# Kernel tuning notes

Measured on AMD Instinct MI355X. Metric: run time of the kernel, lower is better.

Reference implementation:

```python
import jax, jax.numpy as jnp
import numpy as np

B = 65536
NE = 256   # n_encode
NH = 256   # n_hidden
NC = 4     # n_command
D = 64     # n_depth (BatchNorm channels)
F = 32     # n_features
M = D * (F // 2)  # 1024
EPS = 1e-5


def setup_inputs() -> dict:
    key = jax.random.key(0)
    ks = jax.random.split(key, 8)
    s = 0.05
    return {
        "feature": jax.random.normal(ks[0], (B, NE), jnp.float32),
        "hidden":  jax.random.normal(ks[1], (B, NH), jnp.float32),
        "command": jax.random.normal(ks[2], (B, NC), jnp.float32),
        # linear weights (torch Linear stores [out, in]); xavier-like scale
        "Wq":  jax.random.normal(ks[3], (D, NC), jnp.float32) * s,
        "Wkz": jax.random.normal(ks[4], (M, NE), jnp.float32) * s,
        "Wkh": jax.random.normal(ks[5], (M, NH), jnp.float32) * s,
        "Wvz": jax.random.normal(ks[6], (M, NE), jnp.float32) * s,
        "Wvh": jax.random.normal(ks[7], (M, NH), jnp.float32) * s,
        # BatchNorm1d(64) affine params (normV exists in __init__ but is unused)
        "gammaQ": jnp.ones((D,), jnp.float32),
        "betaQ":  jnp.zeros((D,), jnp.float32),
        "gammaK": jnp.ones((D,), jnp.float32),
        "betaK":  jnp.zeros((D,), jnp.float32),
    }


def reference(feature, hidden, command, Wq, Wkz, Wkh, Wvz, Wvh,
              gammaQ, betaQ, gammaK, betaK):
    # Q projection: [B, D]; BatchNorm1d over batch (training-mode batch stats,
    # biased variance, matching torch).
    Q = command @ Wq.T
    mQ = jnp.mean(Q, axis=0)
    vQ = jnp.mean(jnp.square(Q - mQ), axis=0)
    Qn = (Q - mQ) / jnp.sqrt(vQ + EPS) * gammaQ + betaQ          # [B, D]

    # K: cat([B,M],[B,M]) -> [B, 2M] -> view [B, F, D] -> transpose -> [B, D, F]
    K = jnp.concatenate([feature @ Wkz.T, hidden @ Wkh.T], axis=1)
    K = K.reshape(-1, F, D).transpose(0, 2, 1)                    # [B, D, F]
    mK = jnp.mean(K, axis=(0, 2), keepdims=True)
    vK = jnp.mean(jnp.square(K - mK), axis=(0, 2), keepdims=True)
    Kn = (K - mK) / jnp.sqrt(vK + EPS) * gammaK[None, :, None] + betaK[None, :, None]

    # V: [B, F, D], NOT batch-normed (normV is dead code in the original)
    V = jnp.concatenate([feature @ Wvz.T, hidden @ Wvh.T], axis=1).reshape(-1, F, D)

    # attention: [B,1,D] @ [B,D,F] -> [B,F] scores; softmax over F; then @ V
    A = jax.nn.softmax(jnp.einsum('bd,bdf->bf', Qn, Kn) / np.sqrt(D).astype(np.float32), axis=-1)
    s = jnp.einsum('bf,bfd->bd', A, V)                            # [B, D]
    return s
```

## Files before the change

### kernel.cpp

```cpp
#include <hip/hip_runtime.h>
#include <hip/hip_bf16.h>
#include <math.h>


typedef float  f32x4   __attribute__((ext_vector_type(4)));
typedef float  f32x16  __attribute__((ext_vector_type(16)));
typedef __bf16 bf16x4  __attribute__((ext_vector_type(4)));
typedef __bf16 bf16x8  __attribute__((ext_vector_type(8)));

#define MFMA16(A, B, C) __builtin_amdgcn_mfma_f32_16x16x32_bf16((A), (B), (C), 0, 0, 0)
#define MFMA32(A, B, C) __builtin_amdgcn_mfma_f32_32x32x16_bf16((A), (B), (C), 0, 0, 0)

#define EPSV 1e-5f

#define WS_WV    0x000000u
#define WS_WKF   0x100000u
#define WS_G     0x120000u
#define WS_CS    0x1A0000u
#define WS_CMDP  0x1A0800u
#define WS_T     0x1A1800u
#define WS_U     0x1A3800u
#define WS_WQ2   0x1A5800u
#define WS_C0    0x1A5C00u

__device__ __forceinline__ void gl_lds16(const void* g, void* l)
{
    __builtin_amdgcn_global_load_lds(
        (const __attribute__((address_space(1))) unsigned int*)g,
        (__attribute__((address_space(3))) unsigned int*)l, 16, 0, 0);
}

__global__ __launch_bounds__(512, 2) void setup1(const float* __restrict__ feat,
        const float* __restrict__ hid, const float4* __restrict__ cmd,
        const float* __restrict__ Wvz, const float* __restrict__ Wvh,
        __bf16* __restrict__ WV, float* __restrict__ CMDP, float* __restrict__ CS,
        __bf16* __restrict__ Gp)
{
    __shared__ __bf16 T[256 * 40];
    __shared__ float sm[8][14];
    const int blk = blockIdx.x;
    const int tid = threadIdx.x;

    if (blk >= 384) {
        const int b2 = blk - 384;
        float v[14];
#pragma unroll
        for (int k = 0; k < 14; ++k) v[k] = 0.f;
#pragma unroll
        for (int i = 0; i < 4; ++i) {
            float4 c = cmd[(b2 * 4 + i) * 512 + tid];
            v[0] += c.x;  v[1] += c.y;  v[2] += c.z;  v[3] += c.w;
            v[4] += c.x*c.x; v[5] += c.x*c.y; v[6] += c.x*c.z; v[7] += c.x*c.w;
            v[8] += c.y*c.y; v[9] += c.y*c.z; v[10] += c.y*c.w;
            v[11] += c.z*c.z; v[12] += c.z*c.w; v[13] += c.w*c.w;
        }
#pragma unroll
        for (int k = 0; k < 14; ++k) {
            float s = v[k];
#pragma unroll
            for (int off = 32; off; off >>= 1) s += __shfl_xor(s, off);
            if ((tid & 63) == 0) sm[tid >> 6][k] = s;
        }
        __syncthreads();
        if (tid < 14) {
            float s = 0.f;
#pragma unroll
            for (int w = 0; w < 8; ++w) s += sm[w][tid];
            CMDP[b2 * 14 + tid] = s;
        }
        return;
    }
    if (blk >= 128) {
        int t = (blk - 128) * 512 + tid;
        int e = t * 4;
        const float* src = (e < 262144) ? (Wvz + e) : (Wvh + (e - 262144));
        float4 a = *(const float4*)src;
        bf16x4 vv = { (__bf16)a.x, (__bf16)a.y, (__bf16)a.z, (__bf16)a.w };
        *(bf16x4*)(WV + e) = vv;
        return;
    }

    const int mat  = blk >> 6;
    const int chunk = blk & 63;
    const float* X = mat ? hid : feat;
    float* cs = CS + mat * 256;
    const int k0   = chunk * 1024;
    const int wid  = tid >> 6, lane = tid & 63, quad = lane >> 4, l15 = lane & 15;
    const int c    = tid & 255;
    const int t8   = tid >> 8;

    f32x4 acc[2][16];
#pragma unroll
    for (int mt = 0; mt < 2; ++mt)
#pragma unroll
        for (int nt = 0; nt < 16; ++nt) acc[mt][nt] = (f32x4){0.f, 0.f, 0.f, 0.f};

    float clsum = 0.f;
    for (int it = 0; it < 32; ++it) {
        __syncthreads();
        const int kb = k0 + it * 32;
#pragma unroll
        for (int i = 0; i < 16; ++i) {
            int k = t8 + 2 * i;
            float x = X[(size_t)(kb + k) * 256 + c];
            clsum += x;
            T[c * 40 + k] = (__bf16)x;
        }
        __syncthreads();
        bf16x8 a0 = *(const bf16x8*)&T[(wid * 32 +      l15) * 40 + quad * 8];
        bf16x8 a1 = *(const bf16x8*)&T[(wid * 32 + 16 + l15) * 40 + quad * 8];
#pragma unroll
        for (int nt = 0; nt < 16; ++nt) {
            bf16x8 b = *(const bf16x8*)&T[(nt * 16 + l15) * 40 + quad * 8];
            acc[0][nt] = MFMA16(a0, b, acc[0][nt]);
            acc[1][nt] = MFMA16(a1, b, acc[1][nt]);
        }
    }
    atomicAdd(&cs[c], clsum);
    __bf16* outp = Gp + (size_t)blk * 65536;
#pragma unroll
    for (int mt = 0; mt < 2; ++mt)
#pragma unroll
        for (int nt = 0; nt < 16; ++nt)
#pragma unroll
            for (int r = 0; r < 4; ++r) {
                int gi = wid * 32 + mt * 16 + quad * 4 + r;
                int gj = nt * 16 + l15;
                outp[gi * 256 + gj] = (__bf16)acc[mt][nt][r];
            }
}

__global__ void gram_reduce(const __bf16* __restrict__ Gp, float* __restrict__ G)
{
    int o = blockIdx.x * 256 + threadIdx.x;
    int mat = o >> 16, e = o & 65535;
    const __bf16* p = Gp + (size_t)mat * 64 * 65536 + e;
    float s = 0.f;
#pragma unroll 8
    for (int c = 0; c < 64; ++c) s += (float)p[(size_t)c * 65536];
    G[o] = s;
}

__global__ void rowstats(const float* __restrict__ Wkz, const float* __restrict__ Wkh,
        const float* __restrict__ G, const float* __restrict__ CS,
        float* __restrict__ Tout, float* __restrict__ Uout)
{
    const int blk = blockIdx.x;
    const int mat = blk >> 7, jg = blk & 127;
    const float* Wsrc = (mat ? Wkh : Wkz) + (size_t)jg * 8 * 256;
    const float* Gm = G + (size_t)mat * 65536;
    const float* cs = CS + mat * 256;
    __shared__ float wlT[256 * 8];
    __shared__ float red[4][16];
    const int tid = threadIdx.x, wid = tid >> 6, lane = tid & 63;
#pragma unroll
    for (int jj = 0; jj < 8; ++jj) wlT[tid * 8 + jj] = Wsrc[jj * 256 + tid];
    __syncthreads();
    float inner[8];
#pragma unroll
    for (int jj = 0; jj < 8; ++jj) inner[jj] = 0.f;
    for (int r = 0; r < 256; ++r) {
        float g = Gm[r * 256 + tid];
        float4 w0 = *(const float4*)&wlT[r * 8];
        float4 w1 = *(const float4*)&wlT[r * 8 + 4];
        inner[0] = fmaf(w0.x, g, inner[0]); inner[1] = fmaf(w0.y, g, inner[1]);
        inner[2] = fmaf(w0.z, g, inner[2]); inner[3] = fmaf(w0.w, g, inner[3]);
        inner[4] = fmaf(w1.x, g, inner[4]); inner[5] = fmaf(w1.y, g, inner[5]);
        inner[6] = fmaf(w1.z, g, inner[6]); inner[7] = fmaf(w1.w, g, inner[7]);
    }
    float cst = cs[tid];
#pragma unroll
    for (int jj = 0; jj < 8; ++jj) {
        float wme = wlT[tid * 8 + jj];
        float p = wme * inner[jj];
        float u = wme * cst;
#pragma unroll
        for (int off = 32; off; off >>= 1) { p += __shfl_xor(p, off); u += __shfl_xor(u, off); }
        if (lane == 0) { red[wid][jj] = p; red[wid][jj + 8] = u; }
    }
    __syncthreads();
    if (tid < 16) {
        float s = red[0][tid] + red[1][tid] + red[2][tid] + red[3][tid];
        int jj = tid & 7;
        int j = mat * 1024 + jg * 8 + jj;
        if (tid < 8) Tout[j] = s; else Uout[j] = s;
    }
}

__global__ void finalize_kernel(const float* __restrict__ Wq,
        const float* __restrict__ gQ, const float* __restrict__ bQ,
        const float* __restrict__ gK, const float* __restrict__ bK,
        const float* __restrict__ CMDP, const float* __restrict__ T,
        const float* __restrict__ U, float* __restrict__ Wq2, float* __restrict__ C0)
{
    __shared__ float s14[14];
    const int d = threadIdx.x;
    if (d < 14) {
        float s = 0.f;
        for (int b = 0; b < 32; ++b) s += CMDP[b * 14 + d];
        s14[d] = s;
    }
    __syncthreads();
    float s4[4] = { s14[0], s14[1], s14[2], s14[3] };
    float gc[4][4];
    gc[0][0] = s14[4];
    gc[0][1] = gc[1][0] = s14[5];
    gc[0][2] = gc[2][0] = s14[6];
    gc[0][3] = gc[3][0] = s14[7];
    gc[1][1] = s14[8];
    gc[1][2] = gc[2][1] = s14[9];
    gc[1][3] = gc[3][1] = s14[10];
    gc[2][2] = s14[11];
    gc[2][3] = gc[3][2] = s14[12];
    gc[3][3] = s14[13];
    float wq[4];
#pragma unroll
    for (int c = 0; c < 4; ++c) wq[c] = Wq[d * 4 + c];
    const float invB = 1.0f / 65536.0f;
    float mQ = (wq[0]*s4[0] + wq[1]*s4[1] + wq[2]*s4[2] + wq[3]*s4[3]) * invB;
    float eq2 = 0.f;
#pragma unroll
    for (int c = 0; c < 4; ++c)
#pragma unroll
        for (int c2 = 0; c2 < 4; ++c2) eq2 += wq[c] * wq[c2] * gc[c][c2];
    eq2 *= invB;
    float vQ  = eq2 - mQ * mQ;
    float aQ  = gQ[d] / sqrtf(vQ + EPSV);
    float bQv = bQ[d] - mQ * aQ;
    float S2 = 0.f, S1 = 0.f;
#pragma unroll
    for (int f = 0; f < 32; ++f) { S2 += T[f * 64 + d]; S1 += U[f * 64 + d]; }
    const float invBF = 1.0f / (65536.0f * 32.0f);
    float e2 = S2 * invBF, mK = S1 * invBF;
    float vK = e2 - mK * mK;
    float aK = gK[d] / sqrtf(vK + EPSV);
    float c1 = aQ * aK * 0.125f;
    C0[d] = bQv * aK * 0.125f;
#pragma unroll
    for (int c = 0; c < 4; ++c) Wq2[d * 4 + c] = c1 * wq[c];
}

__global__ void foldK(const float* __restrict__ Wkz, const float* __restrict__ Wkh,
                      const float* __restrict__ Wq2, const float* __restrict__ C0,
                      __bf16* __restrict__ WKF)
{
    const int blk = blockIdx.x;
    const int h = blk / 96, rr = blk % 96;
    const int k = threadIdx.x;
    float s = 0.f;
    if (rr < 80) {
        const int c = rr >> 4, fl = rr & 15;
        const float* Wsrc = (h ? Wkh : Wkz) + (size_t)fl * 64 * 256;
        for (int d = 0; d < 64; ++d) {
            float coef = (c == 0) ? C0[d] : Wq2[d * 4 + (c - 1)];
            s = fmaf(coef, Wsrc[d * 256 + k], s);
        }
    }
    WKF[(size_t)(h * 96 + rr) * 256 + k] = (__bf16)s;
}

__global__ __launch_bounds__(256, 2) void fused_attn(
        const float* __restrict__ feat, const float* __restrict__ hid,
        const float4* __restrict__ cmd, const __bf16* __restrict__ WV,
        const __bf16* __restrict__ WKF, float* __restrict__ out)
{
    __shared__ __bf16 BUF[32768];
    __shared__ __bf16 WGTs[16 * 128];
    const int tid  = threadIdx.x;
    const int wid  = tid >> 6, lane = tid & 63;
    const int l5   = lane & 31, hi = lane >> 5;
    const int fl   = l5 & 15;
    const bool low = (l5 < 16);
    const int wrow = (blockIdx.x << 7) + (wid << 5);

    int voff[12];
#pragma unroll
    for (int i = 0; i < 12; ++i) {
        int n = (wid << 1) + (i << 3) + hi;
        voff[i] = n * 256 + ((l5 ^ (n & 7)) << 3);
    }

    float l_i[16];
    f32x16 s_acc[2];
#pragma unroll
    for (int r = 0; r < 16; ++r) { l_i[r] = 0.f; s_acc[0][r] = 0.f; s_acc[1][r] = 0.f; }

    for (int h = 0; h < 2; ++h) {
        const float* X = h ? hid : feat;
        const __bf16* Wkf = WKF + ((size_t)h * 96 << 8);

        bf16x8 a2[16];
#pragma unroll
        for (int u = 0; u < 16; ++u) {
            const float* p = X + ((size_t)(wrow + l5) << 8) + u * 16 + hi * 8;
            float4 x0 = *(const float4*)p;
            float4 x1 = *(const float4*)(p + 4);
            a2[u] = (bf16x8){ (__bf16)x0.x, (__bf16)x0.y, (__bf16)x0.z, (__bf16)x0.w,
                              (__bf16)x1.x, (__bf16)x1.y, (__bf16)x1.z, (__bf16)x1.w };
        }

        __syncthreads();
#pragma unroll
        for (int i = 0; i < 12; ++i)
            gl_lds16(Wkf + voff[i], &BUF[((wid << 1) + (i << 3)) << 8]);
        __syncthreads();

        f32x16 acc1[3];
#pragma unroll
        for (int nt = 0; nt < 3; ++nt)
#pragma unroll
            for (int r = 0; r < 16; ++r) acc1[nt][r] = 0.f;
        __builtin_amdgcn_s_setprio(1);
#pragma unroll
        for (int ks = 0; ks < 16; ++ks)
#pragma unroll
            for (int nt = 0; nt < 3; ++nt) {
                int n = nt * 32 + l5;
                bf16x8 b = *(const bf16x8*)&BUF[n * 256 + (((ks * 2 + hi) ^ (n & 7)) << 3)];
                acc1[nt] = MFMA32(a2[ks], b, acc1[nt]);
            }
        __builtin_amdgcn_s_setprio(0);

#pragma unroll
        for (int g = 0; g < 4; ++g) {
            bf16x4 wv4;
#pragma unroll
            for (int j = 0; j < 4; ++j) {
                const int r = g * 4 + j;
                const int row32 = j + 8 * g + 4 * hi;
                float4 cm = cmd[wrow + row32];
                float e0, e1, t0[3], t1[3];
#pragma unroll
                for (int nt = 0; nt < 3; ++nt) {
                    e0 = acc1[nt][r];
                    e1 = __shfl_xor(e0, 16);
                    t0[nt] = low ? e0 : e1;
                    t1[nt] = low ? e1 : e0;
                }
                float sc = t0[0] + cm.x * t1[0] + cm.y * t0[1]
                                 + cm.z * t1[1] + cm.w * t0[2];
                float w = __expf(sc);
                wv4[j] = (__bf16)w;
                float ws = w;
                ws += __shfl_xor(ws, 1); ws += __shfl_xor(ws, 2);
                ws += __shfl_xor(ws, 4); ws += __shfl_xor(ws, 8);
                l_i[r] += ws;
            }
            if (low) *(bf16x4*)&WGTs[fl * 128 + (wid << 5) + 8 * g + 4 * hi] = wv4;
        }

        __syncthreads();

        {
            const __bf16* base = WV + ((size_t)(h * 16) << 14);
#pragma unroll
            for (int i = 0; i < 8; ++i)
                gl_lds16(base + voff[i], &BUF[((wid << 1) + (i << 3)) << 8]);
        }

        for (int f2 = 0; f2 < 16; ++f2) {
            const int bufsel = (f2 & 1) << 14;
            __syncthreads();
            if (f2 < 15) {
                const __bf16* base = WV + ((size_t)(h * 16 + f2 + 1) << 14);
                const int nsel = bufsel ^ 16384;
#pragma unroll
                for (int i = 0; i < 8; ++i)
                    gl_lds16(base + voff[i], &BUF[nsel + ((((wid << 1) + (i << 3))) << 8)]);
            }
            __builtin_amdgcn_sched_barrier(0);
            f32x16 acc2[2];
#pragma unroll
            for (int r = 0; r < 16; ++r) { acc2[0][r] = 0.f; acc2[1][r] = 0.f; }
            __builtin_amdgcn_s_setprio(1);
#pragma unroll
            for (int ks = 0; ks < 16; ++ks)
#pragma unroll
                for (int nt = 0; nt < 2; ++nt) {
                    int n = nt * 32 + l5;
                    bf16x8 b = *(const bf16x8*)&BUF[bufsel + n * 256
                                                    + (((ks * 2 + hi) ^ (n & 7)) << 3)];
                    acc2[nt] = MFMA32(a2[ks], b, acc2[nt]);
                }
            __builtin_amdgcn_s_setprio(0);
#pragma unroll
            for (int g = 0; g < 4; ++g) {
                bf16x4 wv = *(const bf16x4*)&WGTs[f2 * 128 + (wid << 5) + 8 * g + 4 * hi];
#pragma unroll
                for (int j = 0; j < 4; ++j) {
                    float w = (float)wv[j];
                    s_acc[0][g * 4 + j] += w * acc2[0][g * 4 + j];
                    s_acc[1][g * 4 + j] += w * acc2[1][g * 4 + j];
                }
            }
        }
    }

#pragma unroll
    for (int g = 0; g < 4; ++g)
#pragma unroll
        for (int j = 0; j < 4; ++j) {
            const int r = g * 4 + j;
            float inv = 1.0f / l_i[r];
            size_t row = (size_t)(wrow + j + 8 * g + 4 * hi);
            out[(row << 6) + l5]      = s_acc[0][r] * inv;
            out[(row << 6) + 32 + l5] = s_acc[1][r] * inv;
        }
}

extern "C" void kernel_launch(void* const* d_in, const int* in_sizes, int n_in,
                              void* d_out, int out_size, void* d_ws, size_t ws_size,
                              hipStream_t stream)
{
    (void)in_sizes; (void)n_in; (void)out_size; (void)ws_size;
    const float* feature = (const float*)d_in[0];
    const float* hidden  = (const float*)d_in[1];
    const float* command = (const float*)d_in[2];
    const float* Wq      = (const float*)d_in[3];
    const float* Wkz     = (const float*)d_in[4];
    const float* Wkh     = (const float*)d_in[5];
    const float* Wvz     = (const float*)d_in[6];
    const float* Wvh     = (const float*)d_in[7];
    const float* gammaQ  = (const float*)d_in[8];
    const float* betaQ   = (const float*)d_in[9];
    const float* gammaK  = (const float*)d_in[10];
    const float* betaK   = (const float*)d_in[11];

    char* ws = (char*)d_ws;
    __bf16* WV   = (__bf16*)(ws + WS_WV);
    __bf16* WKF  = (__bf16*)(ws + WS_WKF);
    float*  G    = (float*)(ws + WS_G);
    float*  CS   = (float*)(ws + WS_CS);
    float*  CMDP = (float*)(ws + WS_CMDP);
    float*  Tj   = (float*)(ws + WS_T);
    float*  Uj   = (float*)(ws + WS_U);
    float*  Wq2  = (float*)(ws + WS_WQ2);
    float*  C0   = (float*)(ws + WS_C0);
    float*  outp = (float*)d_out;
    __bf16* Gp   = (__bf16*)d_out;

    hipMemsetAsync(ws + WS_CS, 0, 0x800, stream);
    setup1<<<416, 512, 0, stream>>>(feature, hidden, (const float4*)command,
                                    Wvz, Wvh, WV, CMDP, CS, Gp);
    gram_reduce<<<512, 256, 0, stream>>>(Gp, G);
    rowstats<<<256, 256, 0, stream>>>(Wkz, Wkh, G, CS, Tj, Uj);
    finalize_kernel<<<1, 64, 0, stream>>>(Wq, gammaQ, betaQ, gammaK, betaK,
                                          CMDP, Tj, Uj, Wq2, C0);
    foldK<<<192, 256, 0, stream>>>(Wkz, Wkh, Wq2, C0, WKF);
    fused_attn<<<512, 256, 0, stream>>>(feature, hidden, (const float4*)command,
                                        WV, WKF, outp);
}
```

Measured before the change: 360.3 us.

## Double-buffer Gram tile loads and trim register pressure in fused attention

The Gram-matrix setup kernel now keeps two LDS tiles and two register staging arrays. Global loads for the next k-chunks are issued while MFMAs run on the current tile, so load latency overlaps with compute instead of sitting between barriers. In fused_attn, the precomputed voff offset array is dropped in favour of recomputing offsets inline, and sched_barriers are added around the X loads and the softmax weight stage. These changes aim to lower register pressure and constrain instruction scheduling. The cost is doubled LDS use in setup1 and more registers there for the staged values.

Measured after the change: 337.0 us. 1.07x faster.

```diff
diff --git a/kernel.cpp b/kernel.cpp
--- a/kernel.cpp
+++ b/kernel.cpp
@@ -36,7 +36,7 @@
         __bf16* __restrict__ WV, float* __restrict__ CMDP, float* __restrict__ CS,
         __bf16* __restrict__ Gp)
 {
-    __shared__ __bf16 T[256 * 40];
+    __shared__ __bf16 T[2 * 256 * 40];
     __shared__ float sm[8][14];
     const int blk = blockIdx.x;
     const int tid = threadIdx.x;
@@ -95,27 +95,54 @@
 #pragma unroll
         for (int nt = 0; nt < 16; ++nt) acc[mt][nt] = (f32x4){0.f, 0.f, 0.f, 0.f};
 
+    const float* Xc = X + (size_t)k0 * 256 + c;
+    float ra[16], rb[16];
     float clsum = 0.f;
-    for (int it = 0; it < 32; ++it) {
-        __syncthreads();
-        const int kb = k0 + it * 32;
-#pragma unroll
-        for (int i = 0; i < 16; ++i) {
-            int k = t8 + 2 * i;
-            float x = X[(size_t)(kb + k) * 256 + c];
-            clsum += x;
-            T[c * 40 + k] = (__bf16)x;
-        }
-        __syncthreads();
-        bf16x8 a0 = *(const bf16x8*)&T[(wid * 32 +      l15) * 40 + quad * 8];
-        bf16x8 a1 = *(const bf16x8*)&T[(wid * 32 + 16 + l15) * 40 + quad * 8];
-#pragma unroll
-        for (int nt = 0; nt < 16; ++nt) {
-            bf16x8 b = *(const bf16x8*)&T[(nt * 16 + l15) * 40 + quad * 8];
-            acc[0][nt] = MFMA16(a0, b, acc[0][nt]);
-            acc[1][nt] = MFMA16(a1, b, acc[1][nt]);
-        }
-    }
+
+#define GRAM_LOAD(R, IT) do { \
+        const float* p_ = Xc + (size_t)(IT) * 32 * 256; \
+        _Pragma("unroll") \
+        for (int i_ = 0; i_ < 16; ++i_) (R)[i_] = p_[(size_t)(t8 + 2 * i_) * 256]; \
+    } while (0)
+#define GRAM_WRITE(R, BUFO) do { \
+        _Pragma("unroll") \
+        for (int i_ = 0; i_ < 16; ++i_) { \
+            float x_ = (R)[i_]; clsum += x_; \
+            T[(BUFO) + c * 40 + t8 + 2 * i_] = (__bf16)x_; } \
+    } while (0)
+#define GRAM_MFMA(BUFO) do { \
+        const __bf16* Tb_ = &T[(BUFO)]; \
+        bf16x8 a0_ = *(const bf16x8*)&Tb_[(wid * 32 +      l15) * 40 + quad * 8]; \
+        bf16x8 a1_ = *(const bf16x8*)&Tb_[(wid * 32 + 16 + l15) * 40 + quad * 8]; \
+        _Pragma("unroll") \
+        for (int nt_ = 0; nt_ < 16; ++nt_) { \
+            bf16x8 b_ = *(const bf16x8*)&Tb_[(nt_ * 16 + l15) * 40 + quad * 8]; \
+            acc[0][nt_] = MFMA16(a0_, b_, acc[0][nt_]); \
+            acc[1][nt_] = MFMA16(a1_, b_, acc[1][nt_]); } \
+    } while (0)
+
+    GRAM_LOAD(ra, 0);
+    GRAM_LOAD(rb, 1);
+    GRAM_WRITE(ra, 0);
+    GRAM_LOAD(ra, 2);
+    __syncthreads();
+
+    for (int it2 = 0; it2 < 16; ++it2) {
+        GRAM_WRITE(rb, 10240);
+        if (it2 < 15) GRAM_LOAD(rb, 2 * it2 + 3);
+        GRAM_MFMA(0);
+        __syncthreads();
+        if (it2 < 15) {
+            GRAM_WRITE(ra, 0);
+            if (it2 < 14) GRAM_LOAD(ra, 2 * it2 + 4);
+        }
+        GRAM_MFMA(10240);
+        __syncthreads();
+    }
+#undef GRAM_LOAD
+#undef GRAM_WRITE
+#undef GRAM_MFMA
+
     atomicAdd(&cs[c], clsum);
     __bf16* outp = Gp + (size_t)blk * 65536;
 #pragma unroll
@@ -273,12 +300,11 @@
     const bool low = (l5 < 16);
     const int wrow = (blockIdx.x << 7) + (wid << 5);
 
-    int voff[12];
-#pragma unroll
-    for (int i = 0; i < 12; ++i) {
-        int n = (wid << 1) + (i << 3) + hi;
-        voff[i] = n * 256 + ((l5 ^ (n & 7)) << 3);
-    }
+#define STAGE_CHUNK(SRC, DSTBASE, I) do { \
+        int n_ = (wid << 1) + ((I) << 3) + hi; \
+        gl_lds16((SRC) + n_ * 256 + ((l5 ^ (n_ & 7)) << 3), \
+                 &BUF[(DSTBASE) + (((wid << 1) + ((I) << 3)) << 8)]); \
+    } while (0)
 
     float l_i[16];
     f32x16 s_acc[2];
@@ -297,12 +323,13 @@
             float4 x1 = *(const float4*)(p + 4);
             a2[u] = (bf16x8){ (__bf16)x0.x, (__bf16)x0.y, (__bf16)x0.z, (__bf16)x0.w,
                               (__bf16)x1.x, (__bf16)x1.y, (__bf16)x1.z, (__bf16)x1.w };
+            if ((u & 3) == 3) __builtin_amdgcn_sched_barrier(0);
         }
 
         __syncthreads();
 #pragma unroll
         for (int i = 0; i < 12; ++i)
-            gl_lds16(Wkf + voff[i], &BUF[((wid << 1) + (i << 3)) << 8]);
+            STAGE_CHUNK(Wkf, 0, i);
         __syncthreads();
 
         f32x16 acc1[3];
@@ -347,6 +374,7 @@
                 l_i[r] += ws;
             }
             if (low) *(bf16x4*)&WGTs[fl * 128 + (wid << 5) + 8 * g + 4 * hi] = wv4;
+            __builtin_amdgcn_sched_barrier(0);
         }
 
         __syncthreads();
@@ -355,7 +383,7 @@
             const __bf16* base = WV + ((size_t)(h * 16) << 14);
 #pragma unroll
             for (int i = 0; i < 8; ++i)
-                gl_lds16(base + voff[i], &BUF[((wid << 1) + (i << 3)) << 8]);
+                STAGE_CHUNK(base, 0, i);
         }
 
         for (int f2 = 0; f2 < 16; ++f2) {
@@ -366,7 +394,7 @@
                 const int nsel = bufsel ^ 16384;
 #pragma unroll
                 for (int i = 0; i < 8; ++i)
-                    gl_lds16(base + voff[i], &BUF[nsel + ((((wid << 1) + (i << 3))) << 8)]);
+                    STAGE_CHUNK(base, nsel, i);
             }
             __builtin_amdgcn_sched_barrier(0);
             f32x16 acc2[2];
@@ -395,6 +423,7 @@
             }
         }
     }
+#undef STAGE_CHUNK
 
 #pragma unroll
     for (int g = 0; g < 4; ++g)
```
